# Performance work log

Measured on AMD Instinct MI355X. Metric: run time of the kernel, lower is better.

Reference implementation:

```python
import jax, jax.numpy as jnp
import numpy as np

B, C_FEAT, C_CODE, H, W = 32, 768, 70, 28, 28
FS = 11
NEG = 5
POS_INTRA_SHIFT = 0.18
POS_INTER_SHIFT = 0.12
NEG_INTER_SHIFT = 0.46


def _norm(t):
    # F.normalize(t, dim=1, eps=1e-10)
    n = jnp.sqrt(jnp.sum(t * t, axis=1, keepdims=True))
    return t / jnp.maximum(n, 1e-10)


def _grid_sample(t, coords):
    # torch: F.grid_sample(t, coords.permute(0,2,1,3), padding_mode='border', align_corners=True)
    grid = jnp.transpose(coords, (0, 2, 1, 3))  # [N, Hg, Wg, 2], last dim = (x, y)
    N, C, Hi, Wi = t.shape
    # align_corners=True unnormalize, then border-clip the continuous coordinate
    x = jnp.clip((grid[..., 0] + 1.0) * 0.5 * (Wi - 1), 0.0, Wi - 1.0)
    y = jnp.clip((grid[..., 1] + 1.0) * 0.5 * (Hi - 1), 0.0, Hi - 1.0)
    x0 = jnp.floor(x)
    y0 = jnp.floor(y)
    wx = (x - x0)[:, None]  # broadcast over channel dim
    wy = (y - y0)[:, None]
    x0i = x0.astype(jnp.int32)
    y0i = y0.astype(jnp.int32)
    x1i = jnp.minimum(x0i + 1, Wi - 1)
    y1i = jnp.minimum(y0i + 1, Hi - 1)
    gather = jax.vmap(lambda img, yi, xi: img[:, yi, xi])  # [C,Hg,Wg] per batch elem
    v00 = gather(t, y0i, x0i)
    v01 = gather(t, y0i, x1i)
    v10 = gather(t, y1i, x0i)
    v11 = gather(t, y1i, x1i)
    return (v00 * (1.0 - wx) * (1.0 - wy) + v01 * wx * (1.0 - wy)
            + v10 * (1.0 - wx) * wy + v11 * wx * wy)


def _helper(f1, f2, c1, c2, shift):
    # fd under torch.no_grad -> stop_gradient
    fd = jnp.einsum('nchw,ncij->nhwij', _norm(f1), _norm(f2))
    old_mean = fd.mean()  # pointwise=True branch
    fd = fd - fd.mean(axis=(3, 4), keepdims=True)
    fd = jax.lax.stop_gradient(fd - fd.mean() + old_mean)
    cd = jnp.einsum('nchw,ncij->nhwij', _norm(c1), _norm(c2))
    # zero_clamp=True -> min_val=0.0; stabalize=True -> clamp max 0.8
    loss = -jnp.clip(cd, 0.0, 0.8) * (fd - shift)
    return loss, cd


def _forward(orig_feats, orig_feats_pos, orig_code, orig_code_pos,
             depth_aug_feats, depth_aug_feats_pos, coords1, coords2, perms):
    c1 = coords1 * 2.0 - 1.0
    c2 = coords2 * 2.0 - 1.0
    feats = _grid_sample(orig_feats, c1)
    code = _grid_sample(orig_code, c1)
    feats_pos = _grid_sample(orig_feats_pos, c2)
    code_pos = _grid_sample(orig_code_pos, c2)
    daf = _grid_sample(depth_aug_feats, c1)
    _ = _grid_sample(depth_aug_feats_pos, c2)  # computed (as in torch) but unused

    pos_intra_loss, pos_intra_cd = _helper(daf, daf, code, code, POS_INTRA_SHIFT)
    pos_inter_loss, pos_inter_cd = _helper(feats, feats_pos, code, code_pos, POS_INTER_SHIFT)

    neg_losses, neg_cds = [], []
    for i in range(perms.shape[0]):  # fixed small neg_samples loop
        p = perms[i]
        feats_neg = _grid_sample(orig_feats[p], c2)
        code_neg = _grid_sample(orig_code[p], c2)
        l, cd = _helper(feats, feats_neg, code, code_neg, NEG_INTER_SHIFT)
        neg_losses.append(l)
        neg_cds.append(cd)
    neg_inter_loss = jnp.concatenate(neg_losses, axis=0)
    neg_inter_cd = jnp.concatenate(neg_cds, axis=0)
    return (pos_intra_loss.mean(), pos_intra_cd,
            pos_inter_loss.mean(), pos_inter_cd,
            neg_inter_loss, neg_inter_cd)


def setup_inputs() -> dict:
    key = jax.random.key(0)
    ks = jax.random.split(key, 10)
    rng = np.random.default_rng(0)
    perms = []
    for _ in range(NEG):  # super_perm: derangement-ish permutation
        p = rng.permutation(B)
        p = np.where(p == np.arange(B), p + 1, p) % B
        perms.append(p)
    return {
        'orig_feats': jax.random.normal(ks[0], (B, C_FEAT, H, W), jnp.float32),
        'orig_feats_pos': jax.random.normal(ks[1], (B, C_FEAT, H, W), jnp.float32),
        'orig_salience': jnp.zeros((B, H, W), jnp.float32),
        'orig_salience_pos': jnp.zeros((B, H, W), jnp.float32),
        'orig_code': jax.random.normal(ks[2], (B, C_CODE, H, W), jnp.float32),
        'orig_code_pos': jax.random.normal(ks[3], (B, C_CODE, H, W), jnp.float32),
        'depth_aug_feats': jax.random.normal(ks[4], (B, C_FEAT, H, W), jnp.float32),
        'depth_aug_feats_pos': jax.random.normal(ks[5], (B, C_FEAT, H, W), jnp.float32),
        'coords1': jax.random.uniform(ks[6], (B, FS, FS, 2), jnp.float32),
        'coords2': jax.random.uniform(ks[7], (B, FS, FS, 2), jnp.float32),
        'perms': jnp.asarray(np.stack(perms), dtype=jnp.int32),
    }


def reference(orig_feats, orig_feats_pos, orig_salience, orig_salience_pos,
              orig_code, orig_code_pos, depth_aug_feats, depth_aug_feats_pos,
              coords1, coords2, perms):
    # use_salience=False: salience tensors unused
    return _forward(orig_feats, orig_feats_pos, orig_code, orig_code_pos,
                    depth_aug_feats, depth_aug_feats_pos, coords1, coords2, perms)
```

## Files before the change

### kernel.cpp

```cpp
#include <hip/hip_runtime.h>

#define CF 768
#define CCODE 70
#define NPIX 784
#define P 121
#define NB 32
#define NTOTF 468512.0f

#define OFF_PI_SCALAR 0
#define OFF_PI_CD 1
#define OFF_PO_SCALAR 468513
#define OFF_PO_CD 468514
#define OFF_NEG_LOSS 937026
#define OFF_NEG_CD 3279586

#define WS_BSUMS 0
#define WS_ADDT 768
#define WS_INVF 1024
#define WS_INVC 33792
#define WS_FRAG_FLOAT 62464
#define FEAT_FRAG_SHORTS 98304
#define CODE_FRAG_SHORTS 12288
#define FEATS_TOTAL_SHORTS (8 * 32 * FEAT_FRAG_SHORTS)
#define CODE_BASE_SHORTS FEATS_TOTAL_SHORTS
#define CODE_TOTAL_SHORTS (7 * 32 * CODE_FRAG_SHORTS)
#define WS_NEED2 (WS_FRAG_FLOAT + (FEATS_TOTAL_SHORTS + CODE_TOTAL_SHORTS) / 2)

typedef __attribute__((ext_vector_type(8))) short short8;
typedef __attribute__((ext_vector_type(4))) float f32x4;
typedef unsigned short ushort_t;
typedef unsigned int uint_t;

__device__ __forceinline__ float samp4(const float* __restrict__ img, int c,
                                       const int4 o, const float4 w) {
  const float* p = img + c * NPIX;
  return w.x * p[o.x] + w.y * p[o.y] + w.z * p[o.z] + w.w * p[o.w];
}

__device__ __forceinline__ void mkcoord(const float* cp, int4* o, float4* w) {
  float x = fminf(fmaxf(cp[0] * 27.f, 0.f), 27.f);
  float y = fminf(fmaxf(cp[1] * 27.f, 0.f), 27.f);
  float x0f = floorf(x), y0f = floorf(y);
  int x0 = (int)x0f, y0 = (int)y0f;
  int x1 = min(x0 + 1, 27), y1 = min(y0 + 1, 27);
  float wx = x - x0f, wy = y - y0f;
  *o = make_int4(y0 * 28 + x0, y0 * 28 + x1, y1 * 28 + x0, y1 * 28 + x1);
  *w = make_float4((1.f - wx) * (1.f - wy), wx * (1.f - wy),
                   (1.f - wx) * wy, wx * wy);
}

__device__ __forceinline__ void mkcoord2(const float* cp, int2* o, float4* w) {
  float x = fminf(fmaxf(cp[0] * 27.f, 0.f), 27.f);
  float y = fminf(fmaxf(cp[1] * 27.f, 0.f), 27.f);
  float x0f = floorf(x), y0f = floorf(y);
  int x0 = (int)x0f, y0 = (int)y0f;
  int y1 = min(y0 + 1, 27);
  float wx = x - x0f, wy = y - y0f;
  bool sh = (x0 >= 27);
  int xb = sh ? 26 : x0;
  float wa0 = sh ? 0.f : (1.f - wx) * (1.f - wy);
  float wa1 = sh ? (1.f - wy) : wx * (1.f - wy);
  float wb0 = sh ? 0.f : (1.f - wx) * wy;
  float wb1 = sh ? wy : wx * wy;
  *o = make_int2(y0 * 28 + xb, y1 * 28 + xb);
  *w = make_float4(wa0, wa1, wb0, wb1);
}

__device__ __forceinline__ ushort_t f2bf(float x) {
  uint_t u = __float_as_uint(x);
  u += 0x7fffu + ((u >> 16) & 1u);
  return (ushort_t)(u >> 16);
}

__device__ __forceinline__ float bflo(uint_t u) {
  return __uint_as_float(u << 16);
}
__device__ __forceinline__ float bfhi(uint_t u) {
  return __uint_as_float(u & 0xffff0000u);
}

__global__ __launch_bounds__(256) void presample_img(
    const float* __restrict__ OF, const float* __restrict__ OFP,
    const float* __restrict__ OC, const float* __restrict__ OCP,
    const float* __restrict__ DAF,
    const float* __restrict__ CO1, const float* __restrict__ CO2,
    const int* __restrict__ PERMS, float* __restrict__ ws) {
  ushort_t* frags = (ushort_t*)(ws + WS_FRAG_FLOAT);
  __shared__ float planes[8 * NPIX];
  __shared__ int sh_slot[16], sh_n[16], sh_cb[16];
  __shared__ int sh_ncs;
  const int job = blockIdx.x, tid = threadIdx.x;

  int tensor, m, o;
  if (job < 3072) { tensor = 0; m = job / 96; o = job - m * 96; }
  else if (job < 6144) { int j = job - 3072; tensor = 1; m = j / 96; o = j - m * 96; }
  else if (job < 9216) { int j = job - 6144; tensor = 2; m = j / 96; o = j - m * 96; }
  else if (job < 9600) { int j = job - 9216; tensor = 3; m = j / 12; o = j - m * 12; }
  else { int j = job - 9600; tensor = 4; m = j / 12; o = j - m * 12; }

  const float* src;
  int nch;
  bool feat;
  if (tensor == 0) { src = OF + (size_t)m * CF * NPIX; nch = CF; feat = true; }
  else if (tensor == 1) { src = DAF + (size_t)m * CF * NPIX; nch = CF; feat = true; }
  else if (tensor == 2) { src = OFP + (size_t)m * CF * NPIX; nch = CF; feat = true; }
  else if (tensor == 3) { src = OC + (size_t)m * CCODE * NPIX; nch = CCODE; feat = false; }
  else { src = OCP + (size_t)m * CCODE * NPIX; nch = CCODE; feat = false; }

  if (tid == 0) {
    int cnt = 0;
    if (tensor == 0) {
      sh_slot[0] = 1; sh_n[0] = m; sh_cb[0] = 0; cnt = 1;
      for (int i = 0; i < 5; ++i)
        for (int k = 0; k < NB; ++k)
          if (PERMS[i * NB + k] == m) {
            sh_slot[cnt] = 3 + i; sh_n[cnt] = k; sh_cb[cnt] = 1; ++cnt;
          }
    } else if (tensor == 1) { sh_slot[0] = 0; sh_n[0] = m; sh_cb[0] = 0; cnt = 1; }
    else if (tensor == 2) { sh_slot[0] = 2; sh_n[0] = m; sh_cb[0] = 1; cnt = 1; }
    else if (tensor == 3) {
      sh_slot[0] = 0; sh_n[0] = m; sh_cb[0] = 0; cnt = 1;
      for (int i = 0; i < 5; ++i)
        for (int k = 0; k < NB; ++k)
          if (PERMS[i * NB + k] == m) {
            sh_slot[cnt] = 2 + i; sh_n[cnt] = k; sh_cb[cnt] = 1; ++cnt;
          }
    } else { sh_slot[0] = 1; sh_n[0] = m; sh_cb[0] = 1; cnt = 1; }
    sh_ncs = cnt;
  }

  const int c0 = o * 8;
  {
    int valid = nch - c0;
    valid = valid > 8 ? 8 : (valid < 0 ? 0 : valid);
    const float* sc = src + (size_t)c0 * NPIX;
    const int lim4 = valid * (NPIX / 4);
    for (int e = tid; e < 8 * NPIX / 4; e += 256) {
      float4 v = (e < lim4) ? ((const float4*)sc)[e]
                            : make_float4(0.f, 0.f, 0.f, 0.f);
      ((float4*)planes)[e] = v;
    }
  }
  __syncthreads();

  const int kp = o >> 2, lg = o & 3;
  const int total = sh_ncs * 128;
  for (int s = tid; s < total; s += 256) {
    const int cs = s >> 7, pt = s & 127;
    const int slot = sh_slot[cs], n = sh_n[cs];
    const float* cb = sh_cb[cs] ? CO2 : CO1;
    float v[8];
    if (pt < P) {
      int gi = pt / 11, gj = pt - gi * 11;
      int2 o2;
      float4 w4;
      mkcoord2(cb + (((n * 11 + gj) * 11 + gi) << 1), &o2, &w4);
#pragma unroll
      for (int i = 0; i < 8; ++i) {
        const float* pl = planes + i * NPIX;
        v[i] = w4.x * pl[o2.x] + w4.y * pl[o2.x + 1] + w4.z * pl[o2.y] +
               w4.w * pl[o2.y + 1];
      }
    } else {
#pragma unroll
      for (int i = 0; i < 8; ++i) v[i] = 0.f;
    }
    uint4 q;
    q.x = (uint_t)f2bf(v[0]) | ((uint_t)f2bf(v[1]) << 16);
    q.y = (uint_t)f2bf(v[2]) | ((uint_t)f2bf(v[3]) << 16);
    q.z = (uint_t)f2bf(v[4]) | ((uint_t)f2bf(v[5]) << 16);
    q.w = (uint_t)f2bf(v[6]) | ((uint_t)f2bf(v[7]) << 16);
    size_t fragbase = feat ? (size_t)(slot * 32 + n) * FEAT_FRAG_SHORTS
                           : CODE_BASE_SHORTS + (size_t)(slot * 32 + n) * CODE_FRAG_SHORTS;
    *(uint4*)(frags + fragbase +
              ((size_t)((kp * 8 + (pt >> 4)) * 64 + lg * 16 + (pt & 15)) << 3)) = q;
  }
}

__global__ __launch_bounds__(128) void norms_kernel(float* __restrict__ ws) {
  const ushort_t* frags = (const ushort_t*)(ws + WS_FRAG_FLOAT);
  const int b = blockIdx.x, p = threadIdx.x;
  float s = 0.f;
  if (b < 256) {
    const int slot = b >> 5, n = b & 31;
    const uint4* F = (const uint4*)(frags + (size_t)(slot * 32 + n) * FEAT_FRAG_SHORTS);
    for (int kp = 0; kp < 24; ++kp) {
#pragma unroll
      for (int lg = 0; lg < 4; ++lg) {
        uint4 q = F[(kp * 8 + (p >> 4)) * 64 + lg * 16 + (p & 15)];
        float a;
        a = bflo(q.x); s = fmaf(a, a, s); a = bfhi(q.x); s = fmaf(a, a, s);
        a = bflo(q.y); s = fmaf(a, a, s); a = bfhi(q.y); s = fmaf(a, a, s);
        a = bflo(q.z); s = fmaf(a, a, s); a = bfhi(q.z); s = fmaf(a, a, s);
        a = bflo(q.w); s = fmaf(a, a, s); a = bfhi(q.w); s = fmaf(a, a, s);
      }
    }
    ws[WS_INVF + (slot * 32 + n) * 128 + p] = 1.f / fmaxf(sqrtf(s), 1e-10f);
  } else {
    const int b2 = b - 256;
    const int slot = b2 >> 5, n = b2 & 31;
    const uint4* F = (const uint4*)(frags + CODE_BASE_SHORTS +
                                    (size_t)(slot * 32 + n) * CODE_FRAG_SHORTS);
#pragma unroll
    for (int kp = 0; kp < 3; ++kp) {
#pragma unroll
      for (int lg = 0; lg < 4; ++lg) {
        uint4 q = F[(kp * 8 + (p >> 4)) * 64 + lg * 16 + (p & 15)];
        float a;
        a = bflo(q.x); s = fmaf(a, a, s); a = bfhi(q.x); s = fmaf(a, a, s);
        a = bflo(q.y); s = fmaf(a, a, s); a = bfhi(q.y); s = fmaf(a, a, s);
        a = bflo(q.z); s = fmaf(a, a, s); a = bfhi(q.z); s = fmaf(a, a, s);
        a = bflo(q.w); s = fmaf(a, a, s); a = bfhi(q.w); s = fmaf(a, a, s);
      }
    }
    ws[WS_INVC + (slot * 32 + n) * 128 + p] = 1.f / fmaxf(sqrtf(s), 1e-10f);
  }
}

__global__ __launch_bounds__(256) void gram_mfma(float* __restrict__ ws,
                                                 float* __restrict__ out) {
  const ushort_t* frags = (const ushort_t*)(ws + WS_FRAG_FLOAT);
  const int bid = blockIdx.x, pair = bid >> 5, n = bid & 31;
  const int tid = threadIdx.x, wave = tid >> 6, lane = tid & 63;
  __shared__ float invAf[128], invBf[128], invAc[128], invBc[128];
  __shared__ float red[4][3];
  const int afslot = (pair == 0) ? 0 : 1;
  const int bfslot = (pair == 0) ? 0 : (pair == 1 ? 2 : 3 + (pair - 2));
  const int bcslot = (pair == 0) ? 0 : (pair == 1 ? 1 : 2 + (pair - 2));
  if (tid < 128) {
    invAf[tid] = ws[WS_INVF + (afslot * 32 + n) * 128 + tid];
    invBf[tid] = ws[WS_INVF + (bfslot * 32 + n) * 128 + tid];
    invAc[tid] = ws[WS_INVC + (0 * 32 + n) * 128 + tid];
    invBc[tid] = ws[WS_INVC + (bcslot * 32 + n) * 128 + tid];
  }
  __syncthreads();

  const short8* Af = (const short8*)(frags + (size_t)(afslot * 32 + n) * FEAT_FRAG_SHORTS);
  const short8* Bf = (const short8*)(frags + (size_t)(bfslot * 32 + n) * FEAT_FRAG_SHORTS);

  f32x4 acc[2][8];
#pragma unroll
  for (int j = 0; j < 2; ++j)
#pragma unroll
    for (int t = 0; t < 8; ++t) acc[j][t] = (f32x4){0.f, 0.f, 0.f, 0.f};

#pragma unroll 2
  for (int kp = 0; kp < 24; ++kp) {
    short8 a0 = Af[(kp * 8 + 2 * wave) * 64 + lane];
    short8 a1 = Af[(kp * 8 + 2 * wave + 1) * 64 + lane];
    short8 bv[8];
#pragma unroll
    for (int t = 0; t < 8; ++t) bv[t] = Bf[(kp * 8 + t) * 64 + lane];
#pragma unroll
    for (int t = 0; t < 8; ++t) {
      acc[0][t] = __builtin_amdgcn_mfma_f32_16x16x32_bf16(a0, bv[t], acc[0][t], 0, 0, 0);
      acc[1][t] = __builtin_amdgcn_mfma_f32_16x16x32_bf16(a1, bv[t], acc[1][t], 0, 0, 0);
    }
  }

  const int lane4 = (lane >> 4) << 2;
  const int cl15 = lane & 15;
  float sfd = 0.f;
#pragma unroll
  for (int j = 0; j < 2; ++j) {
    const int rb = (2 * wave + j) * 16 + lane4;
    const float ivr0 = invAf[rb], ivr1 = invAf[rb + 1], ivr2 = invAf[rb + 2],
                ivr3 = invAf[rb + 3];
    float rs0 = 0.f, rs1 = 0.f, rs2 = 0.f, rs3 = 0.f;
#pragma unroll
    for (int t = 0; t < 8; ++t) {
      const float ivc = invBf[t * 16 + cl15];
      float v0 = acc[j][t].x * ivr0 * ivc;
      float v1 = acc[j][t].y * ivr1 * ivc;
      float v2 = acc[j][t].z * ivr2 * ivc;
      float v3 = acc[j][t].w * ivr3 * ivc;
      acc[j][t].x = v0; acc[j][t].y = v1; acc[j][t].z = v2; acc[j][t].w = v3;
      rs0 += v0; rs1 += v1; rs2 += v2; rs3 += v3;
    }
    sfd += rs0 + rs1 + rs2 + rs3;
    rs0 += __shfl_xor(rs0, 1); rs0 += __shfl_xor(rs0, 2);
    rs0 += __shfl_xor(rs0, 4); rs0 += __shfl_xor(rs0, 8);
    rs1 += __shfl_xor(rs1, 1); rs1 += __shfl_xor(rs1, 2);
    rs1 += __shfl_xor(rs1, 4); rs1 += __shfl_xor(rs1, 8);
    rs2 += __shfl_xor(rs2, 1); rs2 += __shfl_xor(rs2, 2);
    rs2 += __shfl_xor(rs2, 4); rs2 += __shfl_xor(rs2, 8);
    rs3 += __shfl_xor(rs3, 1); rs3 += __shfl_xor(rs3, 2);
    rs3 += __shfl_xor(rs3, 4); rs3 += __shfl_xor(rs3, 8);
    const float rm0 = rs0 * (1.f / 121.f), rm1 = rs1 * (1.f / 121.f);
    const float rm2 = rs2 * (1.f / 121.f), rm3 = rs3 * (1.f / 121.f);
#pragma unroll
    for (int t = 0; t < 8; ++t) {
      acc[j][t].x -= rm0; acc[j][t].y -= rm1; acc[j][t].z -= rm2; acc[j][t].w -= rm3;
    }
  }

  int cd_base, loss_base = 0;
  if (pair == 0) cd_base = OFF_PI_CD + n * 14641;
  else if (pair == 1) cd_base = OFF_PO_CD + n * 14641;
  else {
    int t0 = ((pair - 2) * NB + n) * 14641;
    cd_base = OFF_NEG_CD + t0;
    loss_base = OFF_NEG_LOSS + t0;
  }

  if (pair >= 2) {
#pragma unroll
    for (int j = 0; j < 2; ++j) {
      const int rb = (2 * wave + j) * 16 + lane4;
      if (rb < P) {
#pragma unroll
        for (int t = 0; t < 8; ++t) {
          const int c = t * 16 + cl15;
          if (c < P) {
            float* o = out + loss_base + rb * P + c;
            o[0] = acc[j][t].x;
            if (rb + 1 < P) o[P] = acc[j][t].y;
            if (rb + 2 < P) o[2 * P] = acc[j][t].z;
            if (rb + 3 < P) o[3 * P] = acc[j][t].w;
          }
        }
      }
    }
  }

  const short8* Ac = (const short8*)(frags + CODE_BASE_SHORTS + (size_t)n * CODE_FRAG_SHORTS);
  const short8* Bc = (const short8*)(frags + CODE_BASE_SHORTS + (size_t)(bcslot * 32 + n) * CODE_FRAG_SHORTS);
  f32x4 cacc[2][8];
#pragma unroll
  for (int j = 0; j < 2; ++j)
#pragma unroll
    for (int t = 0; t < 8; ++t) cacc[j][t] = (f32x4){0.f, 0.f, 0.f, 0.f};
#pragma unroll
  for (int kp = 0; kp < 3; ++kp) {
    short8 a0 = Ac[(kp * 8 + 2 * wave) * 64 + lane];
    short8 a1 = Ac[(kp * 8 + 2 * wave + 1) * 64 + lane];
    short8 bv[8];
#pragma unroll
    for (int t = 0; t < 8; ++t) bv[t] = Bc[(kp * 8 + t) * 64 + lane];
#pragma unroll
    for (int t = 0; t < 8; ++t) {
      cacc[0][t] = __builtin_amdgcn_mfma_f32_16x16x32_bf16(a0, bv[t], cacc[0][t], 0, 0, 0);
      cacc[1][t] = __builtin_amdgcn_mfma_f32_16x16x32_bf16(a1, bv[t], cacc[1][t], 0, 0, 0);
    }
  }

  float s1 = 0.f, s2 = 0.f;
#pragma unroll
  for (int j = 0; j < 2; ++j) {
    const int rb = (2 * wave + j) * 16 + lane4;
    const float ivr0 = invAc[rb], ivr1 = invAc[rb + 1], ivr2 = invAc[rb + 2],
                ivr3 = invAc[rb + 3];
#pragma unroll
    for (int t = 0; t < 8; ++t) {
      const int c = t * 16 + cl15;
      const float ivc = invBc[c];
      float c0v = cacc[j][t].x * ivr0 * ivc;
      float c1v = cacc[j][t].y * ivr1 * ivc;
      float c2v = cacc[j][t].z * ivr2 * ivc;
      float c3v = cacc[j][t].w * ivr3 * ivc;
      if (c < P && rb < P) {
        float* o = out + cd_base + rb * P + c;
        o[0] = c0v;
        if (rb + 1 < P) o[P] = c1v;
        if (rb + 2 < P) o[2 * P] = c2v;
        if (rb + 3 < P) o[3 * P] = c3v;
      }
      if (pair < 2) {
        float cl0 = fminf(fmaxf(c0v, 0.f), 0.8f);
        float cl1 = fminf(fmaxf(c1v, 0.f), 0.8f);
        float cl2 = fminf(fmaxf(c2v, 0.f), 0.8f);
        float cl3 = fminf(fmaxf(c3v, 0.f), 0.8f);
        s1 = fmaf(cl0, acc[j][t].x, s1);
        s1 = fmaf(cl1, acc[j][t].y, s1);
        s1 = fmaf(cl2, acc[j][t].z, s1);
        s1 = fmaf(cl3, acc[j][t].w, s1);
        s2 += cl0 + cl1 + cl2 + cl3;
      }
    }
  }

#pragma unroll
  for (int m = 1; m < 64; m <<= 1) {
    sfd += __shfl_xor(sfd, m);
    s1 += __shfl_xor(s1, m);
    s2 += __shfl_xor(s2, m);
  }
  if ((tid & 63) == 0) { red[wave][0] = sfd; red[wave][1] = s1; red[wave][2] = s2; }
  __syncthreads();
  if (tid == 0) {
    float a = 0.f, b2 = 0.f, c2 = 0.f;
    for (int w = 0; w < 4; ++w) { a += red[w][0]; b2 += red[w][1]; c2 += red[w][2]; }
    float* bsums = ws + WS_BSUMS;
    bsums[bid * 3 + 0] = a;
    bsums[bid * 3 + 1] = b2;
    bsums[bid * 3 + 2] = c2;
  }
}

__global__ void loss_finish2(float* __restrict__ ws, float* __restrict__ out) {
  __shared__ float s[7][3];
  const float* bsums = ws + WS_BSUMS;
  float* addterm = ws + WS_ADDT;
  int tid = threadIdx.x;
  if (tid < 21) {
    int pr = tid / 3, k = tid % 3;
    float a = 0.f;
    for (int i = 0; i < 32; ++i) a += bsums[(pr * 32 + i) * 3 + k];
    s[pr][k] = a;
  }
  __syncthreads();
  if (tid == 0) {
    const float invN = 1.f / NTOTF;
    out[OFF_PI_SCALAR] = -(s[0][1] + (s[0][0] * invN - 0.18f) * s[0][2]) * invN;
    out[OFF_PO_SCALAR] = -(s[1][1] + (s[1][0] * invN - 0.12f) * s[1][2]) * invN;
  }
  if (tid >= 1 && tid < 6) addterm[tid - 1] = s[tid + 1][0] / NTOTF - 0.46f;
}

__global__ __launch_bounds__(256) void neg_loss_kernel(
    float* __restrict__ lossr, const float* __restrict__ cdr,
    const float* __restrict__ addterm) {
  __shared__ float at[5];
  if (threadIdx.x < 5) at[threadIdx.x] = addterm[threadIdx.x];
  __syncthreads();
  const int total4 = 5 * 117128;
  float4* l4 = (float4*)lossr;
  const float4* c4 = (const float4*)cdr;
  for (int e = blockIdx.x * 256 + threadIdx.x; e < total4; e += gridDim.x * 256) {
    int k = e / 117128;
    float4 cd = c4[e];
    float4 fv = l4[e];
    float a = at[k];
    float4 r;
    r.x = -fminf(fmaxf(cd.x, 0.f), 0.8f) * (fv.x + a);
    r.y = -fminf(fmaxf(cd.y, 0.f), 0.8f) * (fv.y + a);
    r.z = -fminf(fmaxf(cd.z, 0.f), 0.8f) * (fv.z + a);
    r.w = -fminf(fmaxf(cd.w, 0.f), 0.8f) * (fv.w + a);
    l4[e] = r;
  }
}


__global__ __launch_bounds__(256) void loss_main_fb(
    const float* __restrict__ OF, const float* __restrict__ OFP,
    const float* __restrict__ OC, const float* __restrict__ OCP,
    const float* __restrict__ DAF,
    const float* __restrict__ CO1, const float* __restrict__ CO2,
    const int* __restrict__ PERMS,
    float* __restrict__ out, float* __restrict__ bsums) {
  const int b = blockIdx.x;
  const int pair = b >> 7;
  const int rem = b & 127;
  const int n = rem >> 2;
  const int rg = rem & 3;
  const int row_start = rg * 31;
  const int rcount = min(31, P - row_start);
  const int tid = threadIdx.x;
  const int tx = tid & 15, ty = tid >> 4;

  const float *F1, *F2, *C1, *C2, *CB;
  if (pair == 0) {
    F1 = DAF + (size_t)n * CF * NPIX; F2 = F1;
    C1 = OC + (size_t)n * CCODE * NPIX; C2 = C1;
    CB = CO1;
  } else if (pair == 1) {
    F1 = OF + (size_t)n * CF * NPIX; F2 = OFP + (size_t)n * CF * NPIX;
    C1 = OC + (size_t)n * CCODE * NPIX; C2 = OCP + (size_t)n * CCODE * NPIX;
    CB = CO2;
  } else {
    int n2 = PERMS[(pair - 2) * NB + n];
    F1 = OF + (size_t)n * CF * NPIX; F2 = OF + (size_t)n2 * CF * NPIX;
    C1 = OC + (size_t)n * CCODE * NPIX; C2 = OC + (size_t)n2 * CCODE * NPIX;
    CB = CO2;
  }

  __shared__ int4 Bo[P];
  __shared__ float4 Bw[P];
  __shared__ int4 Ao[32];
  __shared__ float4 Aw[32];
  __shared__ float Abuf[CCODE][32];
  __shared__ float Bbuf[CCODE][128];
  __shared__ float invA[32], invB[128];
  __shared__ float red[4][3];

  if (tid < P) {
    int gi = tid / 11, gj = tid - gi * 11;
    const float* cp = CB + (((n * 11 + gj) * 11 + gi) << 1);
    mkcoord(cp, &Bo[tid], &Bw[tid]);
  } else if (tid >= 128 && tid < 160) {
    int r = tid - 128;
    int q = row_start + r;
    if (q < P) {
      int gi = q / 11, gj = q - gi * 11;
      const float* cp = CO1 + (((n * 11 + gj) * 11 + gi) << 1);
      mkcoord(cp, &Ao[r], &Aw[r]);
    }
  }
  __syncthreads();

  float acc[2][2][4];
#pragma unroll
  for (int kr = 0; kr < 2; ++kr)
#pragma unroll
    for (int m = 0; m < 2; ++m)
#pragma unroll
      for (int u = 0; u < 4; ++u) acc[kr][m][u] = 0.f;
  float ansq = 0.f, bnsq = 0.f;

  for (int ch = 0; ch < 12; ++ch) {
    const int c0 = ch * 64;
    if (ch) __syncthreads();
    for (int e = tid; e < 64 * 128; e += 256) {
      int col = e & 127, cc = e >> 7;
      float v = 0.f;
      if (col < P) v = samp4(F2, c0 + cc, Bo[col], Bw[col]);
      Bbuf[cc][col] = v;
    }
    for (int e = tid; e < 64 * 32; e += 256) {
      int col = e & 31, cc = e >> 5;
      float v = 0.f;
      if (col < rcount) v = samp4(F1, c0 + cc, Ao[col], Aw[col]);
      Abuf[cc][col] = v;
    }
    __syncthreads();
    if (tid < 128) {
      float s = 0.f;
      for (int cc = 0; cc < 64; ++cc) { float v = Bbuf[cc][tid]; s = fmaf(v, v, s); }
      bnsq += s;
    } else if (tid < 160) {
      int r = tid - 128;
      float s = 0.f;
      for (int cc = 0; cc < 64; ++cc) { float v = Abuf[cc][r]; s = fmaf(v, v, s); }
      ansq += s;
    }
    for (int cc = 0; cc < 64; ++cc) {
      const float2 av = *(const float2*)&Abuf[cc][ty * 2];
      const float4 b0 = *(const float4*)&Bbuf[cc][tx * 4];
      const float4 b1 = *(const float4*)&Bbuf[cc][tx * 4 + 64];
      float a[2] = {av.x, av.y};
      float bb[2][4] = {{b0.x, b0.y, b0.z, b0.w}, {b1.x, b1.y, b1.z, b1.w}};
#pragma unroll
      for (int kr = 0; kr < 2; ++kr)
#pragma unroll
        for (int m = 0; m < 2; ++m)
#pragma unroll
          for (int u = 0; u < 4; ++u)
            acc[kr][m][u] = fmaf(a[kr], bb[m][u], acc[kr][m][u]);
    }
  }
  __syncthreads();
  if (tid < 128) invB[tid] = (tid < P) ? 1.f / fmaxf(sqrtf(bnsq), 1e-10f) : 0.f;
  else if (tid < 160) {
    int r = tid - 128;
    invA[r] = (r < rcount) ? 1.f / fmaxf(sqrtf(ansq), 1e-10f) : 0.f;
  }
  __syncthreads();

  float ia[2] = {invA[2 * ty], invA[2 * ty + 1]};
  float ib[2][4];
#pragma unroll
  for (int m = 0; m < 2; ++m)
#pragma unroll
    for (int u = 0; u < 4; ++u) ib[m][u] = invB[m * 64 + tx * 4 + u];

  float fdc[2][2][4];
  float sfd = 0.f;
#pragma unroll
  for (int kr = 0; kr < 2; ++kr) {
    float part = 0.f;
#pragma unroll
    for (int m = 0; m < 2; ++m)
#pragma unroll
      for (int u = 0; u < 4; ++u) {
        float v = acc[kr][m][u] * ia[kr] * ib[m][u];
        fdc[kr][m][u] = v;
        part += v;
      }
    sfd += part;
    float rs = part;
#pragma unroll
    for (int s = 1; s < 16; s <<= 1) rs += __shfl_xor(rs, s, 16);
    float rowm = rs * (1.f / 121.f);
#pragma unroll
    for (int m = 0; m < 2; ++m)
#pragma unroll
      for (int u = 0; u < 4; ++u) fdc[kr][m][u] -= rowm;
  }
  __syncthreads();

  for (int e = tid; e < CCODE * 128; e += 256) {
    int col = e & 127, cc = e >> 7;
    float v = 0.f;
    if (col < P) v = samp4(C2, cc, Bo[col], Bw[col]);
    Bbuf[cc][col] = v;
  }
  for (int e = tid; e < CCODE * 32; e += 256) {
    int col = e & 31, cc = e >> 5;
    float v = 0.f;
    if (col < rcount) v = samp4(C1, cc, Ao[col], Aw[col]);
    Abuf[cc][col] = v;
  }
  __syncthreads();
  if (tid < 128) {
    float s = 0.f;
    for (int cc = 0; cc < CCODE; ++cc) { float v = Bbuf[cc][tid]; s = fmaf(v, v, s); }
    invB[tid] = (tid < P) ? 1.f / fmaxf(sqrtf(s), 1e-10f) : 0.f;
  } else if (tid < 160) {
    int r = tid - 128;
    float s = 0.f;
    for (int cc = 0; cc < CCODE; ++cc) { float v = Abuf[cc][r]; s = fmaf(v, v, s); }
    invA[r] = (r < rcount) ? 1.f / fmaxf(sqrtf(s), 1e-10f) : 0.f;
  }
  float cacc[2][2][4];
#pragma unroll
  for (int kr = 0; kr < 2; ++kr)
#pragma unroll
    for (int m = 0; m < 2; ++m)
#pragma unroll
      for (int u = 0; u < 4; ++u) cacc[kr][m][u] = 0.f;
  for (int cc = 0; cc < CCODE; ++cc) {
    const float2 av = *(const float2*)&Abuf[cc][ty * 2];
    const float4 b0 = *(const float4*)&Bbuf[cc][tx * 4];
    const float4 b1 = *(const float4*)&Bbuf[cc][tx * 4 + 64];
    float a[2] = {av.x, av.y};
    float bb[2][4] = {{b0.x, b0.y, b0.z, b0.w}, {b1.x, b1.y, b1.z, b1.w}};
#pragma unroll
    for (int kr = 0; kr < 2; ++kr)
#pragma unroll
      for (int m = 0; m < 2; ++m)
#pragma unroll
        for (int u = 0; u < 4; ++u)
          cacc[kr][m][u] = fmaf(a[kr], bb[m][u], cacc[kr][m][u]);
  }
  __syncthreads();
  float iac[2] = {invA[2 * ty], invA[2 * ty + 1]};
  float ibc[2][4];
#pragma unroll
  for (int m = 0; m < 2; ++m)
#pragma unroll
    for (int u = 0; u < 4; ++u) ibc[m][u] = invB[m * 64 + tx * 4 + u];

  int cd_base, loss_base = 0;
  if (pair == 0) cd_base = OFF_PI_CD + n * 14641;
  else if (pair == 1) cd_base = OFF_PO_CD + n * 14641;
  else {
    int t = ((pair - 2) * NB + n) * 14641;
    cd_base = OFF_NEG_CD + t;
    loss_base = OFF_NEG_LOSS + t;
  }

  float s1 = 0.f, s2 = 0.f;
#pragma unroll
  for (int kr = 0; kr < 2; ++kr) {
    int r = 2 * ty + kr;
    if (r < rcount) {
      int rglob = row_start + r;
#pragma unroll
      for (int m = 0; m < 2; ++m)
#pragma unroll
        for (int u = 0; u < 4; ++u) {
          int c = m * 64 + tx * 4 + u;
          if (c < P) {
            float cdv = cacc[kr][m][u] * iac[kr] * ibc[m][u];
            int idx = rglob * P + c;
            out[cd_base + idx] = cdv;
            float cl = fminf(fmaxf(cdv, 0.f), 0.8f);
            float fv = fdc[kr][m][u];
            if (pair < 2) { s1 = fmaf(cl, fv, s1); s2 += cl; }
            else out[loss_base + idx] = fv;
          }
        }
    }
  }

#pragma unroll
  for (int s = 1; s < 64; s <<= 1) {
    sfd += __shfl_xor(sfd, s);
    s1 += __shfl_xor(s1, s);
    s2 += __shfl_xor(s2, s);
  }
  int wv = tid >> 6;
  if ((tid & 63) == 0) { red[wv][0] = sfd; red[wv][1] = s1; red[wv][2] = s2; }
  __syncthreads();
  if (tid == 0) {
    float a = 0.f, bb = 0.f, cc = 0.f;
    for (int w = 0; w < 4; ++w) { a += red[w][0]; bb += red[w][1]; cc += red[w][2]; }
    bsums[b * 3 + 0] = a;
    bsums[b * 3 + 1] = bb;
    bsums[b * 3 + 2] = cc;
  }
}

__global__ void loss_finish_fb(const float* __restrict__ bsums,
                               float* __restrict__ out,
                               float* __restrict__ addterm) {
  __shared__ float s[7][3];
  int tid = threadIdx.x;
  if (tid < 21) {
    int pr = tid / 3, k = tid % 3;
    float a = 0.f;
    const float* p = bsums + (pr * 128) * 3 + k;
    for (int i = 0; i < 128; ++i) a += p[i * 3];
    s[pr][k] = a;
  }
  __syncthreads();
  if (tid == 0) {
    const float invN = 1.f / NTOTF;
    out[OFF_PI_SCALAR] = -(s[0][1] + (s[0][0] * invN - 0.18f) * s[0][2]) * invN;
    out[OFF_PO_SCALAR] = -(s[1][1] + (s[1][0] * invN - 0.12f) * s[1][2]) * invN;
  }
  if (tid >= 1 && tid < 6) addterm[tid - 1] = s[tid + 1][0] / NTOTF - 0.46f;
}

__global__ __launch_bounds__(256) void neg_loss_fb(
    float* __restrict__ lossr, const float* __restrict__ cdr,
    const float* __restrict__ addterm) {
  __shared__ float at[5];
  if (threadIdx.x < 5) at[threadIdx.x] = addterm[threadIdx.x];
  __syncthreads();
  const int total = 5 * 468512;
  for (int e = blockIdx.x * 256 + threadIdx.x; e < total; e += gridDim.x * 256) {
    int k = e / 468512;
    float cdv = cdr[e];
    float cl = fminf(fmaxf(cdv, 0.f), 0.8f);
    lossr[e] = -cl * (lossr[e] + at[k]);
  }
}

extern "C" void kernel_launch(void* const* d_in, const int* in_sizes, int n_in,
                              void* d_out, int out_size, void* d_ws,
                              size_t ws_size, hipStream_t stream) {
  const float* OF = (const float*)d_in[0];
  const float* OFP = (const float*)d_in[1];
  const float* OC = (const float*)d_in[4];
  const float* OCP = (const float*)d_in[5];
  const float* DAF = (const float*)d_in[6];
  const float* CO1 = (const float*)d_in[8];
  const float* CO2 = (const float*)d_in[9];
  const int* PERMS = (const int*)d_in[10];
  float* out = (float*)d_out;
  float* ws = (float*)d_ws;

  if (ws_size >= (size_t)WS_NEED2 * sizeof(float)) {
    hipLaunchKernelGGL(presample_img, dim3(9984), dim3(256), 0, stream,
                       OF, OFP, OC, OCP, DAF, CO1, CO2, PERMS, ws);
    hipLaunchKernelGGL(norms_kernel, dim3(480), dim3(128), 0, stream, ws);
    hipLaunchKernelGGL(gram_mfma, dim3(224), dim3(256), 0, stream, ws, out);
    hipLaunchKernelGGL(loss_finish2, dim3(1), dim3(64), 0, stream, ws, out);
    hipLaunchKernelGGL(neg_loss_kernel, dim3(1024), dim3(256), 0, stream,
                       out + OFF_NEG_LOSS, out + OFF_NEG_CD, ws + WS_ADDT);
  } else {
    float* bsums = ws;
    float* addterm = bsums + 896 * 3;
    hipLaunchKernelGGL(loss_main_fb, dim3(896), dim3(256), 0, stream,
                       OF, OFP, OC, OCP, DAF, CO1, CO2, PERMS, out, bsums);
    hipLaunchKernelGGL(loss_finish_fb, dim3(1), dim3(64), 0, stream,
                       bsums, out, addterm);
    hipLaunchKernelGGL(neg_loss_fb, dim3(2048), dim3(256), 0, stream,
                       out + OFF_NEG_LOSS, out + OFF_NEG_CD, addterm);
  }
}
```

Baseline: 155.5 us.

## Pipeline channel-octet loads through registers in presample kernel

Each presample block now handles four consecutive 8-channel octets instead of one, cutting the grid by four. The global load of the next octet goes into registers while the current octet is sampled from shared memory, so load latency overlaps with the bilinear sampling work. Each block also parses the perms table once per four octets instead of once per octet. In exchange each thread holds seven float4 registers and there are fewer blocks to hide latency, which may lower occupancy and parallelism.

After: 147.8 us. 5.0% less time.

```diff
diff --git a/kernel.cpp b/kernel.cpp
--- a/kernel.cpp
+++ b/kernel.cpp
@@ -79,7 +79,8 @@
   return __uint_as_float(u & 0xffff0000u);
 }
 
-__global__ __launch_bounds__(256) void presample_img(
+#define GOCT 4
+__global__ __launch_bounds__(256) void presample_pipe(
     const float* __restrict__ OF, const float* __restrict__ OFP,
     const float* __restrict__ OC, const float* __restrict__ OCP,
     const float* __restrict__ DAF,
@@ -91,12 +92,12 @@
   __shared__ int sh_ncs;
   const int job = blockIdx.x, tid = threadIdx.x;
 
-  int tensor, m, o;
-  if (job < 3072) { tensor = 0; m = job / 96; o = job - m * 96; }
-  else if (job < 6144) { int j = job - 3072; tensor = 1; m = j / 96; o = j - m * 96; }
-  else if (job < 9216) { int j = job - 6144; tensor = 2; m = j / 96; o = j - m * 96; }
-  else if (job < 9600) { int j = job - 9216; tensor = 3; m = j / 12; o = j - m * 12; }
-  else { int j = job - 9600; tensor = 4; m = j / 12; o = j - m * 12; }
+  int tensor, m, g0;
+  if (job < 768) { tensor = 0; m = job / 24; g0 = (job - m * 24) * 4; }
+  else if (job < 1536) { int j = job - 768; tensor = 1; m = j / 24; g0 = (j - m * 24) * 4; }
+  else if (job < 2304) { int j = job - 1536; tensor = 2; m = j / 24; g0 = (j - m * 24) * 4; }
+  else if (job < 2400) { int j = job - 2304; tensor = 3; m = j / 3; g0 = (j - m * 3) * 4; }
+  else { int j = job - 2400; tensor = 4; m = j / 3; g0 = (j - m * 3) * 4; }
 
   const float* src;
   int nch;
@@ -129,52 +130,78 @@
     sh_ncs = cnt;
   }
 
-  const int c0 = o * 8;
-  {
-    int valid = nch - c0;
-    valid = valid > 8 ? 8 : (valid < 0 ? 0 : valid);
-    const float* sc = src + (size_t)c0 * NPIX;
-    const int lim4 = valid * (NPIX / 4);
-    for (int e = tid; e < 8 * NPIX / 4; e += 256) {
-      float4 v = (e < lim4) ? ((const float4*)sc)[e]
-                            : make_float4(0.f, 0.f, 0.f, 0.f);
-      ((float4*)planes)[e] = v;
-    }
-  }
-  __syncthreads();
-
-  const int kp = o >> 2, lg = o & 3;
-  const int total = sh_ncs * 128;
-  for (int s = tid; s < total; s += 256) {
-    const int cs = s >> 7, pt = s & 127;
-    const int slot = sh_slot[cs], n = sh_n[cs];
-    const float* cb = sh_cb[cs] ? CO2 : CO1;
-    float v[8];
-    if (pt < P) {
-      int gi = pt / 11, gj = pt - gi * 11;
-      int2 o2;
-      float4 w4;
-      mkcoord2(cb + (((n * 11 + gj) * 11 + gi) << 1), &o2, &w4);
-#pragma unroll
-      for (int i = 0; i < 8; ++i) {
-        const float* pl = planes + i * NPIX;
-        v[i] = w4.x * pl[o2.x] + w4.y * pl[o2.x + 1] + w4.z * pl[o2.y] +
-               w4.w * pl[o2.y + 1];
+  float4 buf0, buf1, buf2, buf3, buf4, buf5, buf6;
+#define LOAD_OCT(OCT)                                                        \
+  {                                                                          \
+    const int c0_ = (OCT) * 8;                                               \
+    int valid_ = nch - c0_;                                                  \
+    valid_ = valid_ > 8 ? 8 : (valid_ < 0 ? 0 : valid_);                     \
+    const int lim4_ = valid_ * (NPIX / 4);                                   \
+    const float4* sc_ = (const float4*)(src + (size_t)c0_ * NPIX);           \
+    int e_;                                                                  \
+    e_ = tid;          buf0 = (e_ < lim4_) ? sc_[e_] : make_float4(0,0,0,0); \
+    e_ = tid + 256;    buf1 = (e_ < lim4_) ? sc_[e_] : make_float4(0,0,0,0); \
+    e_ = tid + 512;    buf2 = (e_ < lim4_) ? sc_[e_] : make_float4(0,0,0,0); \
+    e_ = tid + 768;    buf3 = (e_ < lim4_) ? sc_[e_] : make_float4(0,0,0,0); \
+    e_ = tid + 1024;   buf4 = (e_ < lim4_) ? sc_[e_] : make_float4(0,0,0,0); \
+    e_ = tid + 1280;   buf5 = (e_ < lim4_) ? sc_[e_] : make_float4(0,0,0,0); \
+    e_ = tid + 1536;                                                         \
+    buf6 = (e_ < 1568 && e_ < lim4_) ? sc_[e_] : make_float4(0,0,0,0);       \
+  }
+
+  LOAD_OCT(g0);
+
+  for (int g = 0; g < GOCT; ++g) {
+    const int o = g0 + g;
+    __syncthreads();
+    {
+      float4* pl4 = (float4*)planes;
+      int e;
+      e = tid;        pl4[e] = buf0;
+      e = tid + 256;  pl4[e] = buf1;
+      e = tid + 512;  pl4[e] = buf2;
+      e = tid + 768;  pl4[e] = buf3;
+      e = tid + 1024; pl4[e] = buf4;
+      e = tid + 1280; pl4[e] = buf5;
+      e = tid + 1536; if (e < 1568) pl4[e] = buf6;
+    }
+    __syncthreads();
+    if (g + 1 < GOCT) LOAD_OCT(g0 + g + 1);
+
+    const int kp = o >> 2, lg = o & 3;
+    const int total = sh_ncs * 128;
+    for (int s = tid; s < total; s += 256) {
+      const int cs = s >> 7, pt = s & 127;
+      const int slot = sh_slot[cs], n = sh_n[cs];
+      const float* cb = sh_cb[cs] ? CO2 : CO1;
+      float v[8];
+      if (pt < P) {
+        int gi = pt / 11, gj = pt - gi * 11;
+        int2 o2;
+        float4 w4;
+        mkcoord2(cb + (((n * 11 + gj) * 11 + gi) << 1), &o2, &w4);
+#pragma unroll
+        for (int i = 0; i < 8; ++i) {
+          const float* pl = planes + i * NPIX;
+          v[i] = w4.x * pl[o2.x] + w4.y * pl[o2.x + 1] + w4.z * pl[o2.y] +
+                 w4.w * pl[o2.y + 1];
+        }
+      } else {
+#pragma unroll
+        for (int i = 0; i < 8; ++i) v[i] = 0.f;
       }
-    } else {
-#pragma unroll
-      for (int i = 0; i < 8; ++i) v[i] = 0.f;
-    }
-    uint4 q;
-    q.x = (uint_t)f2bf(v[0]) | ((uint_t)f2bf(v[1]) << 16);
-    q.y = (uint_t)f2bf(v[2]) | ((uint_t)f2bf(v[3]) << 16);
-    q.z = (uint_t)f2bf(v[4]) | ((uint_t)f2bf(v[5]) << 16);
-    q.w = (uint_t)f2bf(v[6]) | ((uint_t)f2bf(v[7]) << 16);
-    size_t fragbase = feat ? (size_t)(slot * 32 + n) * FEAT_FRAG_SHORTS
-                           : CODE_BASE_SHORTS + (size_t)(slot * 32 + n) * CODE_FRAG_SHORTS;
-    *(uint4*)(frags + fragbase +
-              ((size_t)((kp * 8 + (pt >> 4)) * 64 + lg * 16 + (pt & 15)) << 3)) = q;
-  }
+      uint4 q;
+      q.x = (uint_t)f2bf(v[0]) | ((uint_t)f2bf(v[1]) << 16);
+      q.y = (uint_t)f2bf(v[2]) | ((uint_t)f2bf(v[3]) << 16);
+      q.z = (uint_t)f2bf(v[4]) | ((uint_t)f2bf(v[5]) << 16);
+      q.w = (uint_t)f2bf(v[6]) | ((uint_t)f2bf(v[7]) << 16);
+      size_t fragbase = feat ? (size_t)(slot * 32 + n) * FEAT_FRAG_SHORTS
+                             : CODE_BASE_SHORTS + (size_t)(slot * 32 + n) * CODE_FRAG_SHORTS;
+      *(uint4*)(frags + fragbase +
+                ((size_t)((kp * 8 + (pt >> 4)) * 64 + lg * 16 + (pt & 15)) << 3)) = q;
+    }
+  }
+#undef LOAD_OCT
 }
 
 __global__ __launch_bounds__(128) void norms_kernel(float* __restrict__ ws) {
@@ -742,7 +769,7 @@
   float* ws = (float*)d_ws;
 
   if (ws_size >= (size_t)WS_NEED2 * sizeof(float)) {
-    hipLaunchKernelGGL(presample_img, dim3(9984), dim3(256), 0, stream,
+    hipLaunchKernelGGL(presample_pipe, dim3(2496), dim3(256), 0, stream,
                        OF, OFP, OC, OCP, DAF, CO1, CO2, PERMS, ws);
     hipLaunchKernelGGL(norms_kernel, dim3(480), dim3(128), 0, stream, ws);
     hipLaunchKernelGGL(gram_mfma, dim3(224), dim3(256), 0, stream, ws, out);
```

## Restructure presample into multi-quad blocks with register-prefetched channel planes

Applied to the files above, without the earlier changes.

Reworks the presample kernel so each block walks several 4-channel groups instead of one 8-channel group. The next group's planes are prefetched into registers while the current group is bilinearly sampled from shared memory. Group counts differ per tensor to balance work, and the launch shrinks from 9984 to 2560 blocks. This aims to cut per-block setup cost (perm scans, coordinate work) and hide global load latency, but it adds extra barriers and narrower 8-byte stores.

New measurement: 153.5 us. Within noise of the previous version (-1.3%).

```diff
diff --git a/kernel.cpp b/kernel.cpp
--- a/kernel.cpp
+++ b/kernel.cpp
@@ -79,24 +79,24 @@
   return __uint_as_float(u & 0xffff0000u);
 }
 
-__global__ __launch_bounds__(256) void presample_img(
+__global__ __launch_bounds__(256) void presample_q(
     const float* __restrict__ OF, const float* __restrict__ OFP,
     const float* __restrict__ OC, const float* __restrict__ OCP,
     const float* __restrict__ DAF,
     const float* __restrict__ CO1, const float* __restrict__ CO2,
     const int* __restrict__ PERMS, float* __restrict__ ws) {
   ushort_t* frags = (ushort_t*)(ws + WS_FRAG_FLOAT);
-  __shared__ float planes[8 * NPIX];
+  __shared__ float planes[4 * NPIX];
   __shared__ int sh_slot[16], sh_n[16], sh_cb[16];
   __shared__ int sh_ncs;
   const int job = blockIdx.x, tid = threadIdx.x;
 
-  int tensor, m, o;
-  if (job < 3072) { tensor = 0; m = job / 96; o = job - m * 96; }
-  else if (job < 6144) { int j = job - 3072; tensor = 1; m = j / 96; o = j - m * 96; }
-  else if (job < 9216) { int j = job - 6144; tensor = 2; m = j / 96; o = j - m * 96; }
-  else if (job < 9600) { int j = job - 9216; tensor = 3; m = j / 12; o = j - m * 12; }
-  else { int j = job - 9600; tensor = 4; m = j / 12; o = j - m * 12; }
+  int tensor, m, q0, G;
+  if (job < 1536) { tensor = 0; m = job / 48; q0 = (job - m * 48) * 4; G = 4; }
+  else if (job < 1920) { int j = job - 1536; tensor = 1; m = j / 12; q0 = (j - m * 12) * 16; G = 16; }
+  else if (job < 2304) { int j = job - 1920; tensor = 2; m = j / 12; q0 = (j - m * 12) * 16; G = 16; }
+  else if (job < 2496) { int j = job - 2304; tensor = 3; m = j / 6; q0 = (j - m * 6) * 4; G = 4; }
+  else { int j = job - 2496; tensor = 4; m = j / 2; q0 = (j - m * 2) * 12; G = 12; }
 
   const float* src;
   int nch;
@@ -129,52 +129,69 @@
     sh_ncs = cnt;
   }
 
-  const int c0 = o * 8;
-  {
-    int valid = nch - c0;
-    valid = valid > 8 ? 8 : (valid < 0 ? 0 : valid);
-    const float* sc = src + (size_t)c0 * NPIX;
-    const int lim4 = valid * (NPIX / 4);
-    for (int e = tid; e < 8 * NPIX / 4; e += 256) {
-      float4 v = (e < lim4) ? ((const float4*)sc)[e]
-                            : make_float4(0.f, 0.f, 0.f, 0.f);
-      ((float4*)planes)[e] = v;
-    }
-  }
-  __syncthreads();
-
-  const int kp = o >> 2, lg = o & 3;
-  const int total = sh_ncs * 128;
-  for (int s = tid; s < total; s += 256) {
-    const int cs = s >> 7, pt = s & 127;
-    const int slot = sh_slot[cs], n = sh_n[cs];
-    const float* cb = sh_cb[cs] ? CO2 : CO1;
-    float v[8];
-    if (pt < P) {
-      int gi = pt / 11, gj = pt - gi * 11;
-      int2 o2;
-      float4 w4;
-      mkcoord2(cb + (((n * 11 + gj) * 11 + gi) << 1), &o2, &w4);
-#pragma unroll
-      for (int i = 0; i < 8; ++i) {
-        const float* pl = planes + i * NPIX;
-        v[i] = w4.x * pl[o2.x] + w4.y * pl[o2.x + 1] + w4.z * pl[o2.y] +
-               w4.w * pl[o2.y + 1];
+  float4 buf0, buf1, buf2, buf3;
+#define LOAD_Q(Q)                                                            \
+  {                                                                          \
+    const int c0_ = (Q) * 4;                                                 \
+    int valid_ = nch - c0_;                                                  \
+    valid_ = valid_ > 4 ? 4 : (valid_ < 0 ? 0 : valid_);                     \
+    const int lim4_ = valid_ * (NPIX / 4);                                   \
+    const float4* sc_ = (const float4*)(src + (size_t)c0_ * NPIX);           \
+    int e_;                                                                  \
+    e_ = tid;        buf0 = (e_ < lim4_) ? sc_[e_] : make_float4(0,0,0,0);   \
+    e_ = tid + 256;  buf1 = (e_ < lim4_) ? sc_[e_] : make_float4(0,0,0,0);   \
+    e_ = tid + 512;  buf2 = (e_ < lim4_) ? sc_[e_] : make_float4(0,0,0,0);   \
+    e_ = tid + 768;                                                          \
+    buf3 = (e_ < 784 && e_ < lim4_) ? sc_[e_] : make_float4(0,0,0,0);        \
+  }
+
+  LOAD_Q(q0);
+  __syncthreads();
+
+  for (int g = 0; g < G; ++g) {
+    const int q = q0 + g;
+    {
+      float4* pl4 = (float4*)planes;
+      pl4[tid] = buf0;
+      pl4[tid + 256] = buf1;
+      pl4[tid + 512] = buf2;
+      if (tid < 16) pl4[tid + 768] = buf3;
+    }
+    __syncthreads();
+    if (g + 1 < G) LOAD_Q(q0 + g + 1);
+
+    const int kp = q >> 3, lg = (q >> 1) & 3, h = q & 1;
+    const int total = sh_ncs * 128;
+    for (int s = tid; s < total; s += 256) {
+      const int cs = s >> 7, pt = s & 127;
+      const int slot = sh_slot[cs], n = sh_n[cs];
+      const float* cb = sh_cb[cs] ? CO2 : CO1;
+      float v0 = 0.f, v1 = 0.f, v2 = 0.f, v3 = 0.f;
+      if (pt < P) {
+        int gi = pt / 11, gj = pt - gi * 11;
+        int2 o2;
+        float4 w4;
+        mkcoord2(cb + (((n * 11 + gj) * 11 + gi) << 1), &o2, &w4);
+        const float* p0 = planes;
+        const float* p1 = planes + NPIX;
+        const float* p2 = planes + 2 * NPIX;
+        const float* p3 = planes + 3 * NPIX;
+        v0 = w4.x * p0[o2.x] + w4.y * p0[o2.x + 1] + w4.z * p0[o2.y] + w4.w * p0[o2.y + 1];
+        v1 = w4.x * p1[o2.x] + w4.y * p1[o2.x + 1] + w4.z * p1[o2.y] + w4.w * p1[o2.y + 1];
+        v2 = w4.x * p2[o2.x] + w4.y * p2[o2.x + 1] + w4.z * p2[o2.y] + w4.w * p2[o2.y + 1];
+        v3 = w4.x * p3[o2.x] + w4.y * p3[o2.x + 1] + w4.z * p3[o2.y] + w4.w * p3[o2.y + 1];
       }
-    } else {
-#pragma unroll
-      for (int i = 0; i < 8; ++i) v[i] = 0.f;
-    }
-    uint4 q;
-    q.x = (uint_t)f2bf(v[0]) | ((uint_t)f2bf(v[1]) << 16);
-    q.y = (uint_t)f2bf(v[2]) | ((uint_t)f2bf(v[3]) << 16);
-    q.z = (uint_t)f2bf(v[4]) | ((uint_t)f2bf(v[5]) << 16);
-    q.w = (uint_t)f2bf(v[6]) | ((uint_t)f2bf(v[7]) << 16);
-    size_t fragbase = feat ? (size_t)(slot * 32 + n) * FEAT_FRAG_SHORTS
-                           : CODE_BASE_SHORTS + (size_t)(slot * 32 + n) * CODE_FRAG_SHORTS;
-    *(uint4*)(frags + fragbase +
-              ((size_t)((kp * 8 + (pt >> 4)) * 64 + lg * 16 + (pt & 15)) << 3)) = q;
-  }
+      uint2 qq;
+      qq.x = (uint_t)f2bf(v0) | ((uint_t)f2bf(v1) << 16);
+      qq.y = (uint_t)f2bf(v2) | ((uint_t)f2bf(v3) << 16);
+      size_t fragbase = feat ? (size_t)(slot * 32 + n) * FEAT_FRAG_SHORTS
+                             : CODE_BASE_SHORTS + (size_t)(slot * 32 + n) * CODE_FRAG_SHORTS;
+      *(uint2*)(frags + fragbase + kp * 4096 + (pt >> 4) * 512 + lg * 128 +
+                (pt & 15) * 8 + h * 4) = qq;
+    }
+    __syncthreads();
+  }
+#undef LOAD_Q
 }
 
 __global__ __launch_bounds__(128) void norms_kernel(float* __restrict__ ws) {
@@ -742,7 +759,7 @@
   float* ws = (float*)d_ws;
 
   if (ws_size >= (size_t)WS_NEED2 * sizeof(float)) {
-    hipLaunchKernelGGL(presample_img, dim3(9984), dim3(256), 0, stream,
+    hipLaunchKernelGGL(presample_q, dim3(2560), dim3(256), 0, stream,
                        OF, OFP, OC, OCP, DAF, CO1, CO2, PERMS, ws);
     hipLaunchKernelGGL(norms_kernel, dim3(480), dim3(128), 0, stream, ws);
     hipLaunchKernelGGL(gram_mfma, dim3(224), dim3(256), 0, stream, ws, out);
```
